# Kernel optimization log

Hardware: AMD Instinct MI355X
Metric: run time of the kernel (lower is better)

The kernel has to match this reference:

```python
import jax, jax.numpy as jnp
import numpy as np

# dims: L blocks, S cur_seq, M memory_len, B batch, D embed, H heads, IN input_dim
L, S, M, B, D, H, IN = 4, 512, 512, 8, 1024, 16, 128
HD = D // H
GRU_BIAS = 2.0  # config['gru_bias']


def _ln(x, s, b, eps=1e-5):
    mu = x.mean(-1, keepdims=True)
    var = ((x - mu) ** 2).mean(-1, keepdims=True)
    return (x - mu) * jax.lax.rsqrt(var + eps) * s + b


def _pos_emb(full_seq, dim):
    # SinusoidalPE: freqs = arange(0, dim, 2.0); inv = 10000**(-freqs/dim); seq descending
    freqs = jnp.arange(0, dim, 2.0)
    inv = 10000.0 ** (-freqs / dim)
    seq = jnp.arange(full_seq - 1, -1, -1.0)
    ang = seq[:, None] * inv[None, :]
    return jnp.concatenate([jnp.sin(ang), jnp.cos(ang)], axis=-1)  # (F, dim)


def _rel_shift(x):
    # x: (q, k, b, h) -> Transformer-XL relative shift
    q, k, b, h = x.shape
    xp = jnp.pad(x, ((0, 0), (1, 0), (0, 0), (0, 0)))
    return xp.reshape(k + 1, q, b, h)[1:].reshape(q, k, b, h)


def _gru(x, y, Wr, Ur, Wz, Uz, Wg, Ug):
    r = jax.nn.sigmoid(y @ Wr + x @ Ur)
    z = jax.nn.sigmoid(y @ Wz + x @ Uz - GRU_BIAS)
    hcand = jnp.tanh(y @ Wg + (r * x) @ Ug)
    return (1.0 - z) * x + z * hcand


def setup_inputs() -> dict:
    key = jax.random.key(0)
    ks = iter(jax.random.split(key, 64))

    def mat(*shape):
        return jax.random.normal(next(ks), shape, jnp.float32) * (shape[-2] ** -0.5)

    return dict(
        h=jax.random.normal(next(ks), (B, S, IN), jnp.float32),
        memory=jnp.zeros((L, M, B, D), jnp.float32),
        We=mat(IN, D), be=jnp.zeros((D,), jnp.float32),
        ln1_s=jnp.ones((L, D), jnp.float32), ln1_b=jnp.zeros((L, D), jnp.float32),
        ln2_s=jnp.ones((L, D), jnp.float32), ln2_b=jnp.zeros((L, D), jnp.float32),
        Wq=mat(L, D, D), bq=jnp.zeros((L, D), jnp.float32),
        Wk=mat(L, D, D), bk=jnp.zeros((L, D), jnp.float32),
        Wv=mat(L, D, D), bv=jnp.zeros((L, D), jnp.float32),
        Wr=mat(L, D, D), br=jnp.zeros((L, D), jnp.float32),
        Wo=mat(L, D, D), bo=jnp.zeros((L, D), jnp.float32),
        u=jax.random.normal(next(ks), (L, H, HD), jnp.float32) * 0.02,
        vb=jax.random.normal(next(ks), (L, H, HD), jnp.float32) * 0.02,
        gWr=mat(L, 2, D, D), gUr=mat(L, 2, D, D),
        gWz=mat(L, 2, D, D), gUz=mat(L, 2, D, D),
        gWg=mat(L, 2, D, D), gUg=mat(L, 2, D, D),
        fW1=mat(L, D, 4 * D), fb1=jnp.zeros((L, 4 * D), jnp.float32),
        fW2=mat(L, 4 * D, D), fb2=jnp.zeros((L, D), jnp.float32),
    )


def reference(h, memory, We, be, ln1_s, ln1_b, ln2_s, ln2_b,
              Wq, bq, Wk, bk, Wv, bv, Wr, br, Wo, bo, u, vb,
              gWr, gUr, gWz, gUz, gWg, gUg, fW1, fb1, fW2, fb2):
    x = jnp.transpose(h, (1, 0, 2))                      # (S, B, IN)
    x = jax.nn.gelu(x @ We + be, approximate=False)      # (S, B, D)
    F = S + M
    pos = _pos_emb(F, D)                                 # (F, D)
    mask = jnp.triu(jnp.ones((S, F), bool), k=1 + M)     # (S, F)
    scale = HD ** -0.5
    out = x
    for i in range(L):
        full = jnp.concatenate([memory[i], out], axis=0)  # (F, B, D)
        qn = _ln(out, ln1_s[i], ln1_b[i])
        kn = _ln(full, ln1_s[i], ln1_b[i])
        q = (qn @ Wq[i] + bq[i]).reshape(S, B, H, HD)
        k = (kn @ Wk[i] + bk[i]).reshape(F, B, H, HD)
        v = (kn @ Wv[i] + bv[i]).reshape(F, B, H, HD)
        r = (pos @ Wr[i] + br[i]).reshape(F, H, HD)
        content = jnp.einsum('ibhd,jbhd->ijbh', q + u[i], k)
        position = _rel_shift(jnp.einsum('ibhd,jhd->ijbh', q + vb[i], r))
        attn = (content + position) * scale               # (S, F, B, H)
        attn = jnp.where(mask[:, :, None, None], -1e30, attn)
        a = jax.nn.softmax(attn, axis=1)
        y = jnp.einsum('ijbh,jbhd->ibhd', a, v).reshape(S, B, D) @ Wo[i] + bo[i]
        y = jax.nn.gelu(y, approximate=False)
        out1 = _gru(out, y, gWr[i, 0], gUr[i, 0], gWz[i, 0], gUz[i, 0], gWg[i, 0], gUg[i, 0])
        e = _ln(out1, ln2_s[i], ln2_b[i])
        e = jax.nn.gelu(e @ fW1[i] + fb1[i], approximate=False)
        e = jax.nn.gelu(e @ fW2[i] + fb2[i], approximate=False)
        out = _gru(out1, e, gWr[i, 1], gUr[i, 1], gWz[i, 1], gUz[i, 1], gWg[i, 1], gUg[i, 1])
    return jnp.transpose(out, (1, 0, 2))                  # (B, S, D)
```

## Files before the change

kernel.cpp:

```cpp
#include <hip/hip_runtime.h>

typedef unsigned short u16;
typedef unsigned long long u64;
typedef __attribute__((ext_vector_type(8))) short bf16x8;
typedef __attribute__((ext_vector_type(4))) float f32x4;

#define DEVI __device__ __forceinline__

DEVI u16 f2b(float f) {
  unsigned u = __float_as_uint(f);
  u += 0x7fffu + ((u >> 16) & 1u);
  return (u16)(u >> 16);
}
DEVI float b2f(u16 v) { return __uint_as_float((unsigned)v << 16); }
DEVI float tanh_f(float x) {
  float xc = fminf(fmaxf(x, -15.f), 15.f);
  float e = __expf(2.f * xc);
  return (e - 1.f) / (e + 1.f);
}
DEVI float gelu_f(float x) {
  float u = 0.7978845608028654f * x * (1.f + 0.044715f * x * x);
  return 0.5f * x * (1.f + tanh_f(u));
}
DEVI float sigm_f(float x) { return 1.f / (1.f + __expf(-x)); }

DEVI void gload16(const void* g, void* l) {
  __builtin_amdgcn_global_load_lds((__attribute__((address_space(1))) void*)g,
                                   (__attribute__((address_space(3))) void*)l, 16, 0, 0);
}

template <int BN>
__global__ __launch_bounds__(256) void gemm_bt(
    const u16* __restrict__ A, const u16* __restrict__ Bt,
    const float* __restrict__ bias, float* __restrict__ C32, u16* __restrict__ C16,
    int M, int N, int K, int ldA, int ldB, int ldC,
    long long sA, long long sBb, long long sBh, long long sC, int nH, int flags)
{
  constexpr int NF = BN / 32;
  __shared__ __align__(16) u16 Sm[2][(128 + BN) * 64];
  const int z = blockIdx.z;
  const int zb = z / nH, zh = z - zb * nH;
  A  += (long long)z * sA;
  Bt += (long long)zb * sBb + (long long)zh * sBh;
  const long long cOff = (long long)z * sC;
  const int m0 = blockIdx.x * 128, n0 = blockIdx.y * BN;
  const int t = threadIdx.x, lane = t & 63;
  const int wm = ((t >> 7) & 1) * 64, wn = ((t >> 6) & 1) * (BN / 2);

  f32x4 acc[4][NF];
#pragma unroll
  for (int i = 0; i < 4; ++i)
#pragma unroll
    for (int j = 0; j < NF; ++j) { f32x4 zz = {0.f, 0.f, 0.f, 0.f}; acc[i][j] = zz; }

  auto stage = [&](int buf, int k0) {
#pragma unroll
    for (int r = 0; r < 4; ++r) {
      const int c = r * 256 + t;
      const int row = c >> 3;
      const int col = (c & 7) << 3;
      int ga = m0 + row; if (ga >= M) ga = M - 1;
      gload16(A + (long long)ga * ldA + (k0 + col),
              &Sm[buf][(size_t)(r * 256 + (t & 192)) * 8]);
    }
#pragma unroll
    for (int r = 0; r < BN / 32; ++r) {
      const int c = r * 256 + t;
      const int row = c >> 3;
      const int col = (c & 7) << 3;
      int gb = n0 + row; if (gb >= N) gb = N - 1;
      gload16(Bt + (long long)gb * ldB + (k0 + col),
              &Sm[buf][(size_t)(1024 + r * 256 + (t & 192)) * 8]);
    }
  };

  auto compute = [&](int buf) {
    const u16* As = &Sm[buf][0];
    const u16* Bs = &Sm[buf][128 * 64];
#pragma unroll
    for (int ks = 0; ks < 2; ++ks) {
      const int ko = ks * 32 + ((lane >> 4) << 3);
      bf16x8 af[4], bfv[NF];
#pragma unroll
      for (int i = 0; i < 4; ++i)
        af[i] = *(const bf16x8*)&As[(wm + i * 16 + (lane & 15)) * 64 + ko];
#pragma unroll
      for (int i = 0; i < NF; ++i)
        bfv[i] = *(const bf16x8*)&Bs[(wn + i * 16 + (lane & 15)) * 64 + ko];
#pragma unroll
      for (int mi = 0; mi < 4; ++mi)
#pragma unroll
        for (int ni = 0; ni < NF; ++ni)
          acc[mi][ni] = __builtin_amdgcn_mfma_f32_16x16x32_bf16(af[mi], bfv[ni], acc[mi][ni], 0, 0, 0);
    }
  };

  stage(0, 0);
  __syncthreads();
  int cur = 0;
  for (int k0 = 64; k0 < K; k0 += 64) {
    stage(cur ^ 1, k0);
    compute(cur);
    __syncthreads();
    cur ^= 1;
  }
  compute(cur);

  const int cb = n0 + wn + (lane & 15);
  const int rb = m0 + wm + ((lane >> 4) << 2);
#pragma unroll
  for (int ni = 0; ni < NF; ++ni) {
    const int col = cb + ni * 16;
    if (col >= N) continue;
    const float bv = (flags & 2) ? bias[col] : 0.f;
#pragma unroll
    for (int mi = 0; mi < 4; ++mi) {
#pragma unroll
      for (int q = 0; q < 4; ++q) {
        const int row = rb + mi * 16 + q;
        if (row >= M) continue;
        float x = acc[mi][ni][q] + bv;
        if (flags & 1) x = gelu_f(x);
        long long o;
        if (flags & 16)
          o = ((long long)((row & 7) * 16 + (col >> 6)) * ldC + (row >> 3)) * 64 + (col & 63);
        else if (flags & 32)
          o = ((long long)(col >> 6) * 1024 + row) * 64 + (col & 63);
        else
          o = cOff + (long long)row * ldC + col;
        if (flags & 4) C32[o] = x;
        if (flags & 8) C16[o] = f2b(x);
      }
    }
  }
}

__global__ __launch_bounds__(256) void fused_attn(
    const u16* __restrict__ Qu,
    const u16* __restrict__ Qv,
    const u16* __restrict__ Kb,
    const u16* __restrict__ Vt,
    const u16* __restrict__ Rh,
    u16* __restrict__ Y)
{
  constexpr int F = 1024;
  const int bid = blockIdx.x;
  const int wk = (bid & 7) * 128 + (bid >> 3);
  const int i0 = (wk & 7) * 64;
  const int bh = wk >> 3;
  const int h = bh & 15;

  __shared__ __align__(16) u16 QUs[64 * 64];
  __shared__ __align__(16) u16 QVs[64 * 64];
  __shared__ __align__(16) u16 Ks[64 * 64];
  __shared__ __align__(16) u16 Vs[64 * 64];
  __shared__ __align__(16) u16 Rs[64 * 64];
  __shared__ __align__(8) u16 PBT[2][64 * 68];
  __shared__ __align__(16) u16 Ps[4][16][72];

  const int t = threadIdx.x;
  const int lane = t & 63;
  const int wq = t >> 6;
  const int l15 = lane & 15, lhi = lane >> 4;

  const u16* QUg = Qu + ((size_t)bh * 512 + i0) * 64;
  const u16* QVg = Qv + ((size_t)bh * 512 + i0) * 64;
  const u16* Kg = Kb + (size_t)bh * F * 64;
  const u16* Vg = Vt + (size_t)bh * 64 * F;
  const u16* Rg = Rh + (size_t)h * F * 64;

  auto stageT = [&](const u16* g, u16* dst) {
#pragma unroll
    for (int rnd = 0; rnd < 2; ++rnd) {
      const int idx = rnd * 256 + t;
      const int row = idx >> 3;
      const int gs = (idx & 7) ^ (row & 7);
      gload16(g + row * 64 + gs * 8, dst + (size_t)(rnd * 256 + (t & 192)) * 8);
    }
  };
  auto stageVf = [&](int j0) {
#pragma unroll
    for (int rnd = 0; rnd < 2; ++rnd) {
      const int idx = rnd * 256 + t;
      const int row = idx >> 3;
      const int gs = (idx & 7) ^ (row & 7);
      gload16(Vg + (size_t)row * F + j0 + gs * 8, Vs + (size_t)(rnd * 256 + (t & 192)) * 8);
    }
  };

  stageT(QUg, QUs);
  stageT(QVg, QVs);
  const int c_lo0 = 448 - i0;
  stageT(Rg + (size_t)c_lo0 * 64, Rs);
  __syncthreads();
  {
    f32x4 pb0[4];
#pragma unroll
    for (int i = 0; i < 4; ++i) { f32x4 zz = {0.f, 0.f, 0.f, 0.f}; pb0[i] = zz; }
    __builtin_amdgcn_s_setprio(1);
#pragma unroll
    for (int ks = 0; ks < 2; ++ks) {
      const int arow = wq * 16 + l15;
      const bf16x8 av = *(const bf16x8*)&QVs[arow * 64 + (((ks * 4 + lhi) ^ (arow & 7)) << 3)];
#pragma unroll
      for (int ni = 0; ni < 4; ++ni) {
        const int brow = ni * 16 + l15;
        const bf16x8 br_ = *(const bf16x8*)&Rs[brow * 64 + (((ks * 4 + lhi) ^ (brow & 7)) << 3)];
        pb0[ni] = __builtin_amdgcn_mfma_f32_16x16x32_bf16(av, br_, pb0[ni], 0, 0, 0);
      }
    }
    __builtin_amdgcn_s_setprio(0);
#pragma unroll
    for (int ni = 0; ni < 4; ++ni) {
      u64 w = (u64)f2b(pb0[ni][0]) | ((u64)f2b(pb0[ni][1]) << 16) |
              ((u64)f2b(pb0[ni][2]) << 32) | ((u64)f2b(pb0[ni][3]) << 48);
      *(u64*)&PBT[0][(size_t)(ni * 16 + l15) * 68 + wq * 16 + lhi * 4] = w;
    }
  }

  f32x4 Oacc[4];
#pragma unroll
  for (int i = 0; i < 4; ++i) { f32x4 zz = {0.f, 0.f, 0.f, 0.f}; Oacc[i] = zz; }
  float mrow[4] = {-3.0e38f, -3.0e38f, -3.0e38f, -3.0e38f};
  float lrow[4] = {0.f, 0.f, 0.f, 0.f};

  const int nT = i0 / 64 + 9;
  for (int st = 0; st < nT; ++st) {
    const int j0 = st * 64;
    const bool lastT = (st == nT - 1);
    __syncthreads();
    stageT(Kg + (size_t)j0 * 64, Ks);
    stageVf(j0);
    if (!lastT) stageT(Rg + (size_t)(j0 - i0 + 512) * 64, Rs);
    __syncthreads();

    f32x4 cacc[4], pbh[4];
#pragma unroll
    for (int i = 0; i < 4; ++i) {
      f32x4 zz = {0.f, 0.f, 0.f, 0.f};
      cacc[i] = zz; pbh[i] = zz;
    }
    __builtin_amdgcn_s_setprio(1);
#pragma unroll
    for (int ks = 0; ks < 2; ++ks) {
      const int arow = wq * 16 + l15;
      const bf16x8 au = *(const bf16x8*)&QUs[arow * 64 + (((ks * 4 + lhi) ^ (arow & 7)) << 3)];
#pragma unroll
      for (int ni = 0; ni < 4; ++ni) {
        const int brow = ni * 16 + l15;
        const bf16x8 bk_ = *(const bf16x8*)&Ks[brow * 64 + (((ks * 4 + lhi) ^ (brow & 7)) << 3)];
        cacc[ni] = __builtin_amdgcn_mfma_f32_16x16x32_bf16(au, bk_, cacc[ni], 0, 0, 0);
      }
      if (!lastT) {
        const bf16x8 av = *(const bf16x8*)&QVs[arow * 64 + (((ks * 4 + lhi) ^ (arow & 7)) << 3)];
#pragma unroll
        for (int ni = 0; ni < 4; ++ni) {
          const int brow = ni * 16 + l15;
          const bf16x8 br_ = *(const bf16x8*)&Rs[brow * 64 + (((ks * 4 + lhi) ^ (brow & 7)) << 3)];
          pbh[ni] = __builtin_amdgcn_mfma_f32_16x16x32_bf16(av, br_, pbh[ni], 0, 0, 0);
        }
      }
    }
    __builtin_amdgcn_s_setprio(0);

    if (!lastT) {
#pragma unroll
      for (int ni = 0; ni < 4; ++ni) {
        u64 w = (u64)f2b(pbh[ni][0]) | ((u64)f2b(pbh[ni][1]) << 16) |
                ((u64)f2b(pbh[ni][2]) << 32) | ((u64)f2b(pbh[ni][3]) << 48);
        *(u64*)&PBT[(st + 1) & 1][(size_t)(ni * 16 + l15) * 68 + wq * 16 + lhi * 4] = w;
      }
    }

    const int lim = i0 - j0 + 512;
    const u16* pbLo = &PBT[st & 1][0];
    const u16* pbHi = &PBT[(st + 1) & 1][0];
    float sc[4][4];
#pragma unroll
    for (int ni = 0; ni < 4; ++ni) {
      const int dj = ni * 16 + l15;
#pragma unroll
      for (int qq = 0; qq < 4; ++qq) {
        const int di = wq * 16 + lhi * 4 + qq;
        const int cc = dj - di + 63;
        const float pb = b2f((cc < 64) ? pbLo[(size_t)cc * 68 + di]
                                       : pbHi[(size_t)(cc - 64) * 68 + di]);
        float s = (cacc[ni][qq] + pb) * 0.125f;
        if (dj - di > lim) s = -1e30f;
        sc[ni][qq] = s;
      }
    }

    float nm[4], esc[4];
#pragma unroll
    for (int qq = 0; qq < 4; ++qq) {
      float r = fmaxf(fmaxf(sc[0][qq], sc[1][qq]), fmaxf(sc[2][qq], sc[3][qq]));
      r = fmaxf(r, __shfl_xor(r, 1));
      r = fmaxf(r, __shfl_xor(r, 2));
      r = fmaxf(r, __shfl_xor(r, 4));
      r = fmaxf(r, __shfl_xor(r, 8));
      nm[qq] = fmaxf(mrow[qq], r);
      esc[qq] = __expf(mrow[qq] - nm[qq]);
      mrow[qq] = nm[qq];
    }
    float ps[4][4];
    float rsum[4] = {0.f, 0.f, 0.f, 0.f};
#pragma unroll
    for (int ni = 0; ni < 4; ++ni)
#pragma unroll
      for (int qq = 0; qq < 4; ++qq) {
        float p = __expf(sc[ni][qq] - nm[qq]);
        ps[ni][qq] = p;
        rsum[qq] += p;
      }
#pragma unroll
    for (int qq = 0; qq < 4; ++qq) {
      float r = rsum[qq];
      r += __shfl_xor(r, 1);
      r += __shfl_xor(r, 2);
      r += __shfl_xor(r, 4);
      r += __shfl_xor(r, 8);
      lrow[qq] = lrow[qq] * esc[qq] + r;
    }
#pragma unroll
    for (int nd = 0; nd < 4; ++nd)
#pragma unroll
      for (int qq = 0; qq < 4; ++qq) Oacc[nd][qq] *= esc[qq];

#pragma unroll
    for (int ni = 0; ni < 4; ++ni)
#pragma unroll
      for (int qq = 0; qq < 4; ++qq)
        Ps[wq][lhi * 4 + qq][ni * 16 + l15] = f2b(ps[ni][qq]);
    __builtin_amdgcn_s_setprio(1);
#pragma unroll
    for (int ks = 0; ks < 2; ++ks) {
      const bf16x8 pa = *(const bf16x8*)&Ps[wq][l15][ks * 32 + lhi * 8];
#pragma unroll
      for (int nd = 0; nd < 4; ++nd) {
        const int vrow = nd * 16 + l15;
        const bf16x8 vb_ = *(const bf16x8*)&Vs[vrow * 64 + (((ks * 4 + lhi) ^ (vrow & 7)) << 3)];
        Oacc[nd] = __builtin_amdgcn_mfma_f32_16x16x32_bf16(pa, vb_, Oacc[nd], 0, 0, 0);
      }
    }
    __builtin_amdgcn_s_setprio(0);
  }

  float inv[4];
#pragma unroll
  for (int qq = 0; qq < 4; ++qq) inv[qq] = 1.f / lrow[qq];
  const int b = bh >> 4;
#pragma unroll
  for (int nd = 0; nd < 4; ++nd)
#pragma unroll
    for (int qq = 0; qq < 4; ++qq) {
      const int row = i0 + wq * 16 + lhi * 4 + qq;
      const int d = nd * 16 + l15;
      Y[(size_t)row * 8192 + b * 1024 + h * 64 + d] = f2b(Oacc[nd][qq] * inv[qq]);
    }
}

__global__ __launch_bounds__(256) void biasprep(const float* __restrict__ bq,
                                                const float* __restrict__ u,
                                                const float* __restrict__ vb,
                                                float* __restrict__ bqu,
                                                float* __restrict__ dvb)
{
  const int i = blockIdx.x * 256 + threadIdx.x;
  bqu[i] = bq[i] + u[i];
  dvb[i] = vb[i] - u[i];
}

__global__ __launch_bounds__(256) void qv_make(const u16* __restrict__ QU,
                                               const float* __restrict__ dvb,
                                               u16* __restrict__ QV)
{
  const long long idx = (long long)blockIdx.x * 256 + threadIdx.x;
  const int d = idx & 63;
  const int h = (idx >> 15) & 15;
  QV[idx] = f2b(b2f(QU[idx]) + dvb[h * 64 + d]);
}

#define MAXW 20
struct WPack {
  const float* src[MAXW];
  u16* dst[MAXW];
  int K[MAXW], N[MAXW];
  int tilePrefix[MAXW + 1];
  int nm;
};

__global__ __launch_bounds__(256) void wtrans_kernel(WPack p) {
  int bid = blockIdx.x;
  int m = 0;
  while (m < p.nm && bid >= p.tilePrefix[m + 1]) ++m;
  if (m >= p.nm) return;
  const int lt = bid - p.tilePrefix[m];
  const int K = p.K[m], N = p.N[m];
  const int tN = N >> 5;
  const int kt = lt / tN, nt = lt - kt * tN;
  const int k0 = kt << 5, n0 = nt << 5;
  const float* src = p.src[m];
  u16* dst = p.dst[m];
  __shared__ float tile[32][33];
  const int t = threadIdx.x;
  const int r = t >> 3, c4 = (t & 7) << 2;
  float4 v = *(const float4*)&src[(size_t)(k0 + r) * N + n0 + c4];
  tile[r][c4 + 0] = v.x; tile[r][c4 + 1] = v.y; tile[r][c4 + 2] = v.z; tile[r][c4 + 3] = v.w;
  __syncthreads();
  u16 o0 = f2b(tile[c4 + 0][r]);
  u16 o1 = f2b(tile[c4 + 1][r]);
  u16 o2 = f2b(tile[c4 + 2][r]);
  u16 o3 = f2b(tile[c4 + 3][r]);
  u64 w = (u64)o0 | ((u64)o1 << 16) | ((u64)o2 << 32) | ((u64)o3 << 48);
  *(u64*)&dst[(size_t)(n0 + r) * K + k0 + c4] = w;
}

__global__ __launch_bounds__(256) void ln_kernel(
    const float* __restrict__ Xmem, const float* __restrict__ Xout, int rowsMem,
    const float* __restrict__ sc, const float* __restrict__ bi, u16* __restrict__ dst)
{
  const int row = blockIdx.x;
  const float* src = (row < rowsMem) ? (Xmem + (long long)row * 1024)
                                     : (Xout + (long long)(row - rowsMem) * 1024);
  const int t = threadIdx.x;
  float4 v = *(const float4*)&src[t * 4];
  float s1 = v.x + v.y + v.z + v.w;
  float s2 = v.x * v.x + v.y * v.y + v.z * v.z + v.w * v.w;
#pragma unroll
  for (int o = 32; o > 0; o >>= 1) { s1 += __shfl_down(s1, o); s2 += __shfl_down(s2, o); }
  __shared__ float red[8];
  const int wv = t >> 6;
  if ((t & 63) == 0) { red[wv * 2] = s1; red[wv * 2 + 1] = s2; }
  __syncthreads();
  s1 = red[0] + red[2] + red[4] + red[6];
  s2 = red[1] + red[3] + red[5] + red[7];
  const float mu = s1 * (1.f / 1024.f);
  const float var = s2 * (1.f / 1024.f) - mu * mu;
  const float rs = rsqrtf(var + 1e-5f);
  float vals[4] = {v.x, v.y, v.z, v.w};
  u16 o4[4];
#pragma unroll
  for (int j = 0; j < 4; ++j) {
    const int c = t * 4 + j;
    o4[j] = f2b((vals[j] - mu) * rs * sc[c] + bi[c]);
  }
  *(u64*)&dst[(long long)row * 1024 + t * 4] =
      (u64)o4[0] | ((u64)o4[1] << 16) | ((u64)o4[2] << 32) | ((u64)o4[3] << 48);
}

__global__ __launch_bounds__(256) void prep_vt16(const u16* __restrict__ Vf, u16* __restrict__ VT)
{
  const int f0 = blockIdx.x * 64;
  const int bh = blockIdx.y;
  const int b = bh >> 4, h = bh & 15;
  __shared__ u16 tl[64 * 64];
  const int t = threadIdx.x;
  {
    const int fr = t >> 2, c0 = (t & 3) * 16;
    const u16* src = Vf + ((size_t)(f0 + fr) * 8 + b) * 1024 + h * 64 + c0;
    *(bf16x8*)&tl[fr * 64 + c0] = *(const bf16x8*)src;
    *(bf16x8*)&tl[fr * 64 + c0 + 8] = *(const bf16x8*)(src + 8);
  }
  __syncthreads();
  {
    const int dr = t >> 2, c0 = (t & 3) * 16;
    u16* dst = VT + ((long long)bh * 64 + dr) * 1024 + f0 + c0;
#pragma unroll
    for (int j = 0; j < 16; ++j) dst[j] = tl[(c0 + j) * 64 + dr];
  }
}

__global__ __launch_bounds__(256) void pe_kernel(u16* __restrict__ PEB)
{
  const long long idx = (long long)blockIdx.x * 256 + threadIdx.x;
  const int p = (int)(idx >> 10);
  const int d = idx & 1023;
  const int q = d & 511;
  const float inv = powf(10000.f, -(float)(2 * q) * (1.f / 1024.f));
  const float ang = (float)(1023 - p) * inv;
  PEB[idx] = f2b((d < 512) ? sinf(ang) : cosf(ang));
}

__global__ __launch_bounds__(256) void embed_conv(const float* __restrict__ h, u16* __restrict__ A)
{
  const long long idx = (long long)blockIdx.x * 256 + threadIdx.x;
  const int c = idx & 127;
  const int r = (int)(idx >> 7);
  const int s = r >> 3, b = r & 7;
  A[idx] = f2b(h[(((long long)b * 512 + s) << 7) + c]);
}

__global__ __launch_bounds__(256) void gru_elemA(const float* __restrict__ T1, float* __restrict__ T2,
                                                 const float* __restrict__ X, u16* __restrict__ RXBF)
{
  const long long i4 = ((long long)blockIdx.x * 256 + threadIdx.x) * 4;
  const int row = (int)(i4 >> 10);
  const int c = i4 & 1023;
  const float* t1 = T1 + (long long)row * 3072 + c;
  float* t2 = T2 + (long long)row * 2048 + c;
  float4 ry = *(const float4*)t1;
  float4 zy = *(const float4*)(t1 + 1024);
  float4 rx = *(const float4*)t2;
  float4 zx = *(const float4*)(t2 + 1024);
  float4 x = *(const float4*)(X + i4);
  float rr[4], zz[4];
  rr[0] = sigm_f(ry.x + rx.x); rr[1] = sigm_f(ry.y + rx.y);
  rr[2] = sigm_f(ry.z + rx.z); rr[3] = sigm_f(ry.w + rx.w);
  zz[0] = sigm_f(zy.x + zx.x - 2.f); zz[1] = sigm_f(zy.y + zx.y - 2.f);
  zz[2] = sigm_f(zy.z + zx.z - 2.f); zz[3] = sigm_f(zy.w + zx.w - 2.f);
  u16 o4[4];
  o4[0] = f2b(rr[0] * x.x); o4[1] = f2b(rr[1] * x.y);
  o4[2] = f2b(rr[2] * x.z); o4[3] = f2b(rr[3] * x.w);
  *(u64*)&RXBF[i4] = (u64)o4[0] | ((u64)o4[1] << 16) | ((u64)o4[2] << 32) | ((u64)o4[3] << 48);
  float4 zo; zo.x = zz[0]; zo.y = zz[1]; zo.z = zz[2]; zo.w = zz[3];
  *(float4*)t2 = zo;
}

__global__ __launch_bounds__(256) void gru_elemB(const float* __restrict__ T1, const float* __restrict__ T2,
                                                 const float* __restrict__ TG, const float* __restrict__ X,
                                                 float* __restrict__ O, u16* __restrict__ XBF)
{
  const long long i4 = ((long long)blockIdx.x * 256 + threadIdx.x) * 4;
  const int row = (int)(i4 >> 10);
  const int c = i4 & 1023;
  float4 gy = *(const float4*)(T1 + (long long)row * 3072 + 2048 + c);
  float4 tt = *(const float4*)(TG + i4);
  float4 z = *(const float4*)(T2 + (long long)row * 2048 + c);
  float4 x = *(const float4*)(X + i4);
  float4 o;
  o.x = (1.f - z.x) * x.x + z.x * tanh_f(gy.x + tt.x);
  o.y = (1.f - z.y) * x.y + z.y * tanh_f(gy.y + tt.y);
  o.z = (1.f - z.z) * x.z + z.z * tanh_f(gy.z + tt.z);
  o.w = (1.f - z.w) * x.w + z.w * tanh_f(gy.w + tt.w);
  *(float4*)(O + i4) = o;
  u16 o4[4];
  o4[0] = f2b(o.x); o4[1] = f2b(o.y); o4[2] = f2b(o.z); o4[3] = f2b(o.w);
  *(u64*)&XBF[i4] = (u64)o4[0] | ((u64)o4[1] << 16) | ((u64)o4[2] << 32) | ((u64)o4[3] << 48);
}

__global__ __launch_bounds__(256) void out_transpose(const float* __restrict__ O, float* __restrict__ dst)
{
  const long long i4 = ((long long)blockIdx.x * 256 + threadIdx.x) * 4;
  const int d = i4 & 1023;
  const int r = (int)(i4 >> 10);
  const int s = r >> 3, b = r & 7;
  float4 v = *(const float4*)(O + i4);
  *(float4*)&dst[(((long long)b * 512 + s) << 10) + d] = v;
}

extern "C" void kernel_launch(void* const* d_in, const int* in_sizes, int n_in,
                              void* d_out, int out_size, void* d_ws, size_t ws_size,
                              hipStream_t stream)
{
  (void)in_sizes; (void)n_in; (void)out_size; (void)ws_size;
  const float* h_in   = (const float*)d_in[0];
  const float* memory = (const float*)d_in[1];
  const float* We     = (const float*)d_in[2];
  const float* be     = (const float*)d_in[3];
  const float* ln1s   = (const float*)d_in[4];
  const float* ln1b   = (const float*)d_in[5];
  const float* ln2s   = (const float*)d_in[6];
  const float* ln2b   = (const float*)d_in[7];
  const float* Wq     = (const float*)d_in[8];
  const float* bq     = (const float*)d_in[9];
  const float* Wk     = (const float*)d_in[10];
  const float* bk     = (const float*)d_in[11];
  const float* Wv     = (const float*)d_in[12];
  const float* bv     = (const float*)d_in[13];
  const float* Wr     = (const float*)d_in[14];
  const float* br     = (const float*)d_in[15];
  const float* Wo     = (const float*)d_in[16];
  const float* bo     = (const float*)d_in[17];
  const float* uu     = (const float*)d_in[18];
  const float* vbp    = (const float*)d_in[19];
  const float* gWr    = (const float*)d_in[20];
  const float* gUr    = (const float*)d_in[21];
  const float* gWz    = (const float*)d_in[22];
  const float* gUz    = (const float*)d_in[23];
  const float* gWg    = (const float*)d_in[24];
  const float* gUg    = (const float*)d_in[25];
  const float* fW1    = (const float*)d_in[26];
  const float* fb1    = (const float*)d_in[27];
  const float* fW2    = (const float*)d_in[28];
  const float* fb2    = (const float*)d_in[29];

  constexpr int S = 512, MM = 512, B = 8, D = 1024, H = 16, IN = 128, F = 1024;
  constexpr int SB = 4096, FB = 8192;
  constexpr long long DD = (long long)D * D;

  char* ws = (char*)d_ws;
  size_t off = 0;
  auto alloc = [&](size_t bytes) -> size_t {
    size_t o = off; off = (off + bytes + 255) & ~(size_t)255; return o;
  };
  const size_t oWT   = alloc((size_t)25 * DD * 2);
  const size_t oWET  = alloc((size_t)D * IN * 2);
  const size_t oPEB  = alloc((size_t)F * D * 2);
  const size_t oOUT  = alloc((size_t)SB * D * 4);
  const size_t oOUT1 = alloc((size_t)SB * D * 4);
  const size_t oXBF  = alloc((size_t)SB * D * 2);
  const size_t oYBF  = alloc((size_t)SB * D * 2);
  const size_t oYBFA = alloc((size_t)SB * D * 2);
  const size_t oABUF = alloc((size_t)SB * D * 2);
  const size_t oKN   = alloc((size_t)FB * D * 2);
  const size_t oQU   = alloc((size_t)B * H * S * 64 * 2);
  const size_t oQV   = alloc((size_t)B * H * S * 64 * 2);
  const size_t oKBH  = alloc((size_t)B * H * F * 64 * 2);
  const size_t oVT   = alloc((size_t)B * H * F * 64 * 2);
  const size_t oRH   = alloc((size_t)H * F * 64 * 2);
  const size_t oBQU  = alloc((size_t)D * 4);
  const size_t oDVB  = alloc((size_t)D * 4);
  const size_t oUNI  = off;

  u16* WTp   = (u16*)(ws + oWT);
  u16* WETp  = (u16*)(ws + oWET);
  u16* PEBp  = (u16*)(ws + oPEB);
  float* OUTp  = (float*)(ws + oOUT);
  float* OUT1p = (float*)(ws + oOUT1);
  u16* XBFp  = (u16*)(ws + oXBF);
  u16* YBFp  = (u16*)(ws + oYBF);
  u16* YBFAp = (u16*)(ws + oYBFA);
  u16* ABUFp = (u16*)(ws + oABUF);
  u16* KNp   = (u16*)(ws + oKN);
  u16* QUp   = (u16*)(ws + oQU);
  u16* QVp   = (u16*)(ws + oQV);
  u16* KBHp  = (u16*)(ws + oKBH);
  u16* VTp   = (u16*)(ws + oVT);
  u16* RHp   = (u16*)(ws + oRH);
  float* bquP = (float*)(ws + oBQU);
  float* dvbP = (float*)(ws + oDVB);
  u16* VF16p  = (u16*)(ws + oUNI);
  float* T1   = (float*)(ws + oUNI);
  float* T2   = (float*)(ws + oUNI + (size_t)SB * 3 * D * 4);
  float* TGp  = (float*)(ws + oUNI + (size_t)SB * 5 * D * 4);
  u16* FFNBp  = (u16*)(ws + oUNI);

  auto gemm = [&](const u16* A, const u16* Bt, const float* bias, float* C32, u16* C16,
                  int M, int N, int K, int ldA, int ldB, int ldC,
                  long long sA, long long sBb, long long sBh, long long sC, int nH, int Z,
                  int flags) {
    if (N <= 1024) {
      dim3 grid((M + 127) / 128, (N + 63) / 64, Z);
      gemm_bt<64><<<grid, 256, 0, stream>>>(A, Bt, bias, C32, C16, M, N, K, ldA, ldB, ldC,
                                            sA, sBb, sBh, sC, nH, flags);
    } else {
      dim3 grid((M + 127) / 128, (N + 127) / 128, Z);
      gemm_bt<128><<<grid, 256, 0, stream>>>(A, Bt, bias, C32, C16, M, N, K, ldA, ldB, ldC,
                                             sA, sBb, sBh, sC, nH, flags);
    }
  };

  pe_kernel<<<(F * D) / 256, 256, 0, stream>>>(PEBp);
  {
    WPack p{};
    p.nm = 1; p.src[0] = We; p.dst[0] = WETp; p.K[0] = IN; p.N[0] = D;
    p.tilePrefix[0] = 0; p.tilePrefix[1] = (IN / 32) * (D / 32);
    wtrans_kernel<<<p.tilePrefix[1], 256, 0, stream>>>(p);
  }
  embed_conv<<<(SB * IN) / 256, 256, 0, stream>>>(h_in, ABUFp);
  gemm(ABUFp, WETp, be, OUTp, XBFp, SB, D, IN, IN, IN, D, 0, 0, 0, 0, 1, 1, 1 | 2 | 4 | 8);

  for (int li = 0; li < 4; ++li) {
    WPack p{};
    int nt = 0, id = 0;
    auto addw = [&](const float* s, u16* d, int K, int N) {
      p.src[id] = s; p.dst[id] = d; p.K[id] = K; p.N[id] = N;
      p.tilePrefix[id] = nt; nt += (K / 32) * (N / 32); ++id;
    };
    addw(Wq + li * DD, WTp + 0 * DD, D, D);
    addw(Wk + li * DD, WTp + 1 * DD, D, D);
    addw(Wv + li * DD, WTp + 2 * DD, D, D);
    addw(Wr + li * DD, WTp + 3 * DD, D, D);
    addw(Wo + li * DD, WTp + 4 * DD, D, D);
    addw(gWr + (li * 2 + 0) * DD, WTp + 5 * DD, D, D);
    addw(gWz + (li * 2 + 0) * DD, WTp + 6 * DD, D, D);
    addw(gWg + (li * 2 + 0) * DD, WTp + 7 * DD, D, D);
    addw(gUr + (li * 2 + 0) * DD, WTp + 8 * DD, D, D);
    addw(gUz + (li * 2 + 0) * DD, WTp + 9 * DD, D, D);
    addw(gUg + (li * 2 + 0) * DD, WTp + 10 * DD, D, D);
    addw(gWr + (li * 2 + 1) * DD, WTp + 11 * DD, D, D);
    addw(gWz + (li * 2 + 1) * DD, WTp + 12 * DD, D, D);
    addw(gWg + (li * 2 + 1) * DD, WTp + 13 * DD, D, D);
    addw(gUr + (li * 2 + 1) * DD, WTp + 14 * DD, D, D);
    addw(gUz + (li * 2 + 1) * DD, WTp + 15 * DD, D, D);
    addw(gUg + (li * 2 + 1) * DD, WTp + 16 * DD, D, D);
    addw(fW1 + li * (long long)D * 4096, WTp + 17 * DD, D, 4096);
    addw(fW2 + li * (long long)4096 * D, WTp + 21 * DD, 4096, D);
    p.tilePrefix[id] = nt; p.nm = id;
    wtrans_kernel<<<nt, 256, 0, stream>>>(p);

    ln_kernel<<<FB, 256, 0, stream>>>(memory + (long long)li * MM * B * D, OUTp, MM * B,
                                      ln1s + li * D, ln1b + li * D, KNp);
    const u16* QN = KNp + (size_t)MM * B * D;

    biasprep<<<4, 256, 0, stream>>>(bq + li * D, uu + li * D, vbp + li * D, bquP, dvbP);
    gemm(QN, WTp + 0 * DD, bquP, nullptr, QUp, SB, D, D, D, D,  S,
         0, 0, 0, 0, 1, 1, 2 | 8 | 16);
    qv_make<<<(B * H * S * 64) / 256, 256, 0, stream>>>(QUp, dvbP, QVp);
    gemm(KNp, WTp + 1 * DD, bk + li * D, nullptr, KBHp, FB, D, D, D, D,  F,
         0, 0, 0, 0, 1, 1, 2 | 8 | 16);
    gemm(KNp, WTp + 2 * DD, bv + li * D, nullptr, VF16p, FB, D, D, D, D, D,
         0, 0, 0, 0, 1, 1, 2 | 8);
    prep_vt16<<<dim3(F / 64, B * H), 256, 0, stream>>>(VF16p, VTp);
    gemm(PEBp, WTp + 3 * DD, br + li * D, nullptr, RHp, F, D, D, D, D, D,
         0, 0, 0, 0, 1, 1, 2 | 8 | 32);

    fused_attn<<<dim3((S / 64) * B * H), 256, 0, stream>>>(QUp, QVp, KBHp, VTp, RHp, YBFAp);

    gemm(YBFAp, WTp + 4 * DD, bo + li * D, nullptr, YBFp, SB, D, D, D, D, D, 0, 0, 0, 0, 1, 1, 1 | 2 | 8);

    gemm(YBFp, WTp + 5 * DD, nullptr, T1, nullptr, SB, 3 * D, D, D, D, 3 * D, 0, 0, 0, 0, 1, 1, 4);
    gemm(XBFp, WTp + 8 * DD, nullptr, T2, nullptr, SB, 2 * D, D, D, D, 2 * D, 0, 0, 0, 0, 1, 1, 4);
    gru_elemA<<<(SB * D / 4) / 256, 256, 0, stream>>>(T1, T2, OUTp, ABUFp);
    gemm(ABUFp, WTp + 10 * DD, nullptr, TGp, nullptr, SB, D, D, D, D, D, 0, 0, 0, 0, 1, 1, 4);
    gru_elemB<<<(SB * D / 4) / 256, 256, 0, stream>>>(T1, T2, TGp, OUTp, OUT1p, XBFp);

    ln_kernel<<<SB, 256, 0, stream>>>(OUT1p, OUT1p, SB, ln2s + li * D, ln2b + li * D, ABUFp);
    gemm(ABUFp, WTp + 17 * DD, fb1 + li * 4096, nullptr, FFNBp, SB, 4096, D, D, D, 4096,
         0, 0, 0, 0, 1, 1, 1 | 2 | 8);
    gemm(FFNBp, WTp + 21 * DD, fb2 + li * D, nullptr, YBFp, SB, D, 4096, 4096, 4096, D,
         0, 0, 0, 0, 1, 1, 1 | 2 | 8);

    gemm(YBFp, WTp + 11 * DD, nullptr, T1, nullptr, SB, 3 * D, D, D, D, 3 * D, 0, 0, 0, 0, 1, 1, 4);
    gemm(XBFp, WTp + 14 * DD, nullptr, T2, nullptr, SB, 2 * D, D, D, D, 2 * D, 0, 0, 0, 0, 1, 1, 4);
    gru_elemA<<<(SB * D / 4) / 256, 256, 0, stream>>>(T1, T2, OUT1p, ABUFp);
    gemm(ABUFp, WTp + 16 * DD, nullptr, TGp, nullptr, SB, D, D, D, D, D, 0, 0, 0, 0, 1, 1, 4);
    gru_elemB<<<(SB * D / 4) / 256, 256, 0, stream>>>(T1, T2, TGp, OUT1p, OUTp, XBFp);
  }

  out_transpose<<<(SB * D / 4) / 256, 256, 0, stream>>>(OUTp, (float*)d_out);
}
```

Before: 3.141 ms.

## Double-buffer attention K/V/R tiles and fuse QV and K/V projection GEMMs

The fused attention kernel now double-buffers the K, V and R tiles in shared memory so the loads for the next tile overlap compute on the current one. Q fragments are held in registers instead of shared memory, and the softmax uses exp2 with the log2e factor folded into the scale. On the host side, the qv_make kernel is removed because the Q GEMM epilogue writes both QU and QV, and the K and V projections run as one batched GEMM launch with per-z bias and output selection. These changes cut launches and intermediate traffic but add epilogue branching and more shared-memory use per block.

New measurement: 3.289 ms. +4.7%, slower.

```diff
diff --git a/kernel.cpp b/kernel.cpp
--- a/kernel.cpp
+++ b/kernel.cpp
@@ -32,7 +32,8 @@
 template <int BN>
 __global__ __launch_bounds__(256) void gemm_bt(
     const u16* __restrict__ A, const u16* __restrict__ Bt,
-    const float* __restrict__ bias, float* __restrict__ C32, u16* __restrict__ C16,
+    const float* __restrict__ bias, const float* __restrict__ bias2,
+    float* __restrict__ C32, u16* __restrict__ C16, u16* __restrict__ C16b,
     int M, int N, int K, int ldA, int ldB, int ldC,
     long long sA, long long sBb, long long sBh, long long sC, int nH, int flags)
 {
@@ -112,7 +113,8 @@
   for (int ni = 0; ni < NF; ++ni) {
     const int col = cb + ni * 16;
     if (col >= N) continue;
-    const float bv = (flags & 2) ? bias[col] : 0.f;
+    float bv = 0.f;
+    if (flags & 2) bv = ((flags & 128) && zh) ? bias2[col] : bias[col];
 #pragma unroll
     for (int mi = 0; mi < 4; ++mi) {
 #pragma unroll
@@ -121,15 +123,28 @@
         if (row >= M) continue;
         float x = acc[mi][ni][q] + bv;
         if (flags & 1) x = gelu_f(x);
-        long long o;
-        if (flags & 16)
-          o = ((long long)((row & 7) * 16 + (col >> 6)) * ldC + (row >> 3)) * 64 + (col & 63);
-        else if (flags & 32)
-          o = ((long long)(col >> 6) * 1024 + row) * 64 + (col & 63);
-        else
-          o = cOff + (long long)row * ldC + col;
-        if (flags & 4) C32[o] = x;
-        if (flags & 8) C16[o] = f2b(x);
+        if (flags & 64) {
+          const long long o = ((long long)((row & 7) * 16 + (col >> 6)) * ldC + (row >> 3)) * 64 + (col & 63);
+          C16[o] = f2b(x);
+          C16b[o] = f2b(x + bias2[col]);
+        } else if (flags & 128) {
+          if (zh == 0) {
+            const long long o = ((long long)((row & 7) * 16 + (col >> 6)) * ldC + (row >> 3)) * 64 + (col & 63);
+            C16[o] = f2b(x);
+          } else {
+            C16b[(long long)row * 1024 + col] = f2b(x);
+          }
+        } else {
+          long long o;
+          if (flags & 16)
+            o = ((long long)((row & 7) * 16 + (col >> 6)) * ldC + (row >> 3)) * 64 + (col & 63);
+          else if (flags & 32)
+            o = ((long long)(col >> 6) * 1024 + row) * 64 + (col & 63);
+          else
+            o = cOff + (long long)row * ldC + col;
+          if (flags & 4) C32[o] = x;
+          if (flags & 8) C16[o] = f2b(x);
+        }
       }
     }
   }
@@ -144,17 +159,16 @@
     u16* __restrict__ Y)
 {
   constexpr int F = 1024;
+  constexpr float KSC = 0.1803368801111244f;
   const int bid = blockIdx.x;
   const int wk = (bid & 7) * 128 + (bid >> 3);
   const int i0 = (wk & 7) * 64;
   const int bh = wk >> 3;
   const int h = bh & 15;
 
-  __shared__ __align__(16) u16 QUs[64 * 64];
-  __shared__ __align__(16) u16 QVs[64 * 64];
-  __shared__ __align__(16) u16 Ks[64 * 64];
-  __shared__ __align__(16) u16 Vs[64 * 64];
-  __shared__ __align__(16) u16 Rs[64 * 64];
+  __shared__ __align__(16) u16 Ks[2][64 * 64];
+  __shared__ __align__(16) u16 Vs[2][64 * 64];
+  __shared__ __align__(16) u16 Rs[2][64 * 64];
   __shared__ __align__(8) u16 PBT[2][64 * 68];
   __shared__ __align__(16) u16 Ps[4][16][72];
 
@@ -169,6 +183,14 @@
   const u16* Vg = Vt + (size_t)bh * 64 * F;
   const u16* Rg = Rh + (size_t)h * F * 64;
 
+  bf16x8 au[2], av[2];
+#pragma unroll
+  for (int ks = 0; ks < 2; ++ks) {
+    const int arow = wq * 16 + l15;
+    au[ks] = *(const bf16x8*)(QUg + arow * 64 + ks * 32 + lhi * 8);
+    av[ks] = *(const bf16x8*)(QVg + arow * 64 + ks * 32 + lhi * 8);
+  }
+
   auto stageT = [&](const u16* g, u16* dst) {
 #pragma unroll
     for (int rnd = 0; rnd < 2; ++rnd) {
@@ -178,20 +200,22 @@
       gload16(g + row * 64 + gs * 8, dst + (size_t)(rnd * 256 + (t & 192)) * 8);
     }
   };
-  auto stageVf = [&](int j0) {
+  auto stageVf = [&](int j0, u16* dst) {
 #pragma unroll
     for (int rnd = 0; rnd < 2; ++rnd) {
       const int idx = rnd * 256 + t;
       const int row = idx >> 3;
       const int gs = (idx & 7) ^ (row & 7);
-      gload16(Vg + (size_t)row * F + j0 + gs * 8, Vs + (size_t)(rnd * 256 + (t & 192)) * 8);
+      gload16(Vg + (size_t)row * F + j0 + gs * 8, dst + (size_t)(rnd * 256 + (t & 192)) * 8);
     }
   };
 
-  stageT(QUg, QUs);
-  stageT(QVg, QVs);
-  const int c_lo0 = 448 - i0;
-  stageT(Rg + (size_t)c_lo0 * 64, Rs);
+  const int nT = i0 / 64 + 9;
+
+  stageT(Kg, Ks[0]);
+  stageVf(0, Vs[0]);
+  stageT(Rg + (size_t)(512 - i0) * 64, Rs[0]);
+  stageT(Rg + (size_t)(448 - i0) * 64, Rs[1]);
   __syncthreads();
   {
     f32x4 pb0[4];
@@ -199,16 +223,13 @@
     for (int i = 0; i < 4; ++i) { f32x4 zz = {0.f, 0.f, 0.f, 0.f}; pb0[i] = zz; }
     __builtin_amdgcn_s_setprio(1);
 #pragma unroll
-    for (int ks = 0; ks < 2; ++ks) {
-      const int arow = wq * 16 + l15;
-      const bf16x8 av = *(const bf16x8*)&QVs[arow * 64 + (((ks * 4 + lhi) ^ (arow & 7)) << 3)];
+    for (int ks = 0; ks < 2; ++ks)
 #pragma unroll
       for (int ni = 0; ni < 4; ++ni) {
         const int brow = ni * 16 + l15;
-        const bf16x8 br_ = *(const bf16x8*)&Rs[brow * 64 + (((ks * 4 + lhi) ^ (brow & 7)) << 3)];
-        pb0[ni] = __builtin_amdgcn_mfma_f32_16x16x32_bf16(av, br_, pb0[ni], 0, 0, 0);
+        const bf16x8 br_ = *(const bf16x8*)&Rs[1][brow * 64 + (((ks * 4 + lhi) ^ (brow & 7)) << 3)];
+        pb0[ni] = __builtin_amdgcn_mfma_f32_16x16x32_bf16(av[ks], br_, pb0[ni], 0, 0, 0);
       }
-    }
     __builtin_amdgcn_s_setprio(0);
 #pragma unroll
     for (int ni = 0; ni < 4; ++ni) {
@@ -217,6 +238,7 @@
       *(u64*)&PBT[0][(size_t)(ni * 16 + l15) * 68 + wq * 16 + lhi * 4] = w;
     }
   }
+  __syncthreads();
 
   f32x4 Oacc[4];
 #pragma unroll
@@ -224,15 +246,17 @@
   float mrow[4] = {-3.0e38f, -3.0e38f, -3.0e38f, -3.0e38f};
   float lrow[4] = {0.f, 0.f, 0.f, 0.f};
 
-  const int nT = i0 / 64 + 9;
   for (int st = 0; st < nT; ++st) {
-    const int j0 = st * 64;
+    const int b = st & 1;
     const bool lastT = (st == nT - 1);
-    __syncthreads();
-    stageT(Kg + (size_t)j0 * 64, Ks);
-    stageVf(j0);
-    if (!lastT) stageT(Rg + (size_t)(j0 - i0 + 512) * 64, Rs);
-    __syncthreads();
+
+    if (!lastT) {
+      const int j1 = (st + 1) * 64;
+      stageT(Kg + (size_t)j1 * 64, Ks[b ^ 1]);
+      stageVf(j1, Vs[b ^ 1]);
+      if (st + 1 < nT - 1)
+        stageT(Rg + (size_t)(j1 - i0 + 512) * 64, Rs[b ^ 1]);
+    }
 
     f32x4 cacc[4], pbh[4];
 #pragma unroll
@@ -243,21 +267,18 @@
     __builtin_amdgcn_s_setprio(1);
 #pragma unroll
     for (int ks = 0; ks < 2; ++ks) {
-      const int arow = wq * 16 + l15;
-      const bf16x8 au = *(const bf16x8*)&QUs[arow * 64 + (((ks * 4 + lhi) ^ (arow & 7)) << 3)];
 #pragma unroll
       for (int ni = 0; ni < 4; ++ni) {
         const int brow = ni * 16 + l15;
-        const bf16x8 bk_ = *(const bf16x8*)&Ks[brow * 64 + (((ks * 4 + lhi) ^ (brow & 7)) << 3)];
-        cacc[ni] = __builtin_amdgcn_mfma_f32_16x16x32_bf16(au, bk_, cacc[ni], 0, 0, 0);
+        const bf16x8 bk_ = *(const bf16x8*)&Ks[b][brow * 64 + (((ks * 4 + lhi) ^ (brow & 7)) << 3)];
+        cacc[ni] = __builtin_amdgcn_mfma_f32_16x16x32_bf16(au[ks], bk_, cacc[ni], 0, 0, 0);
       }
       if (!lastT) {
-        const bf16x8 av = *(const bf16x8*)&QVs[arow * 64 + (((ks * 4 + lhi) ^ (arow & 7)) << 3)];
 #pragma unroll
         for (int ni = 0; ni < 4; ++ni) {
           const int brow = ni * 16 + l15;
-          const bf16x8 br_ = *(const bf16x8*)&Rs[brow * 64 + (((ks * 4 + lhi) ^ (brow & 7)) << 3)];
-          pbh[ni] = __builtin_amdgcn_mfma_f32_16x16x32_bf16(av, br_, pbh[ni], 0, 0, 0);
+          const bf16x8 br_ = *(const bf16x8*)&Rs[b][brow * 64 + (((ks * 4 + lhi) ^ (brow & 7)) << 3)];
+          pbh[ni] = __builtin_amdgcn_mfma_f32_16x16x32_bf16(av[ks], br_, pbh[ni], 0, 0, 0);
         }
       }
     }
@@ -272,7 +293,6 @@
       }
     }
 
-    const int lim = i0 - j0 + 512;
     const u16* pbLo = &PBT[st & 1][0];
     const u16* pbHi = &PBT[(st + 1) & 1][0];
     float sc[4][4];
@@ -285,8 +305,8 @@
         const int cc = dj - di + 63;
         const float pb = b2f((cc < 64) ? pbLo[(size_t)cc * 68 + di]
                                        : pbHi[(size_t)(cc - 64) * 68 + di]);
-        float s = (cacc[ni][qq] + pb) * 0.125f;
-        if (dj - di > lim) s = -1e30f;
+        float s = (cacc[ni][qq] + pb) * KSC;
+        if (lastT && dj > di) s = -1e30f;
         sc[ni][qq] = s;
       }
     }
@@ -300,7 +320,7 @@
       r = fmaxf(r, __shfl_xor(r, 4));
       r = fmaxf(r, __shfl_xor(r, 8));
       nm[qq] = fmaxf(mrow[qq], r);
-      esc[qq] = __expf(mrow[qq] - nm[qq]);
+      esc[qq] = exp2f(mrow[qq] - nm[qq]);
       mrow[qq] = nm[qq];
     }
     float ps[4][4];
@@ -309,7 +329,7 @@
     for (int ni = 0; ni < 4; ++ni)
 #pragma unroll
       for (int qq = 0; qq < 4; ++qq) {
-        float p = __expf(sc[ni][qq] - nm[qq]);
+        float p = exp2f(sc[ni][qq] - nm[qq]);
         ps[ni][qq] = p;
         rsum[qq] += p;
       }
@@ -339,11 +359,13 @@
 #pragma unroll
       for (int nd = 0; nd < 4; ++nd) {
         const int vrow = nd * 16 + l15;
-        const bf16x8 vb_ = *(const bf16x8*)&Vs[vrow * 64 + (((ks * 4 + lhi) ^ (vrow & 7)) << 3)];
+        const bf16x8 vb_ = *(const bf16x8*)&Vs[b][vrow * 64 + (((ks * 4 + lhi) ^ (vrow & 7)) << 3)];
         Oacc[nd] = __builtin_amdgcn_mfma_f32_16x16x32_bf16(pa, vb_, Oacc[nd], 0, 0, 0);
       }
     }
     __builtin_amdgcn_s_setprio(0);
+
+    __syncthreads();
   }
 
   float inv[4];
@@ -369,16 +391,6 @@
   const int i = blockIdx.x * 256 + threadIdx.x;
   bqu[i] = bq[i] + u[i];
   dvb[i] = vb[i] - u[i];
-}
-
-__global__ __launch_bounds__(256) void qv_make(const u16* __restrict__ QU,
-                                               const float* __restrict__ dvb,
-                                               u16* __restrict__ QV)
-{
-  const long long idx = (long long)blockIdx.x * 256 + threadIdx.x;
-  const int d = idx & 63;
-  const int h = (idx >> 15) & 15;
-  QV[idx] = f2b(b2f(QU[idx]) + dvb[h * 64 + d]);
 }
 
 #define MAXW 20
@@ -636,17 +648,20 @@
   float* TGp  = (float*)(ws + oUNI + (size_t)SB * 5 * D * 4);
   u16* FFNBp  = (u16*)(ws + oUNI);
 
-  auto gemm = [&](const u16* A, const u16* Bt, const float* bias, float* C32, u16* C16,
+  auto gemm = [&](const u16* A, const u16* Bt, const float* bias, const float* bias2,
+                  float* C32, u16* C16, u16* C16b,
                   int M, int N, int K, int ldA, int ldB, int ldC,
                   long long sA, long long sBb, long long sBh, long long sC, int nH, int Z,
                   int flags) {
     if (N <= 1024) {
       dim3 grid((M + 127) / 128, (N + 63) / 64, Z);
-      gemm_bt<64><<<grid, 256, 0, stream>>>(A, Bt, bias, C32, C16, M, N, K, ldA, ldB, ldC,
+      gemm_bt<64><<<grid, 256, 0, stream>>>(A, Bt, bias, bias2, C32, C16, C16b,
+                                            M, N, K, ldA, ldB, ldC,
                                             sA, sBb, sBh, sC, nH, flags);
     } else {
       dim3 grid((M + 127) / 128, (N + 127) / 128, Z);
-      gemm_bt<128><<<grid, 256, 0, stream>>>(A, Bt, bias, C32, C16, M, N, K, ldA, ldB, ldC,
+      gemm_bt<128><<<grid, 256, 0, stream>>>(A, Bt, bias, bias2, C32, C16, C16b,
+                                             M, N, K, ldA, ldB, ldC,
                                              sA, sBb, sBh, sC, nH, flags);
     }
   };
@@ -659,7 +674,8 @@
     wtrans_kernel<<<p.tilePrefix[1], 256, 0, stream>>>(p);
   }
   embed_conv<<<(SB * IN) / 256, 256, 0, stream>>>(h_in, ABUFp);
-  gemm(ABUFp, WETp, be, OUTp, XBFp, SB, D, IN, IN, IN, D, 0, 0, 0, 0, 1, 1, 1 | 2 | 4 | 8);
+  gemm(ABUFp, WETp, be, nullptr, OUTp, XBFp, nullptr, SB, D, IN, IN, IN, D,
+       0, 0, 0, 0, 1, 1, 1 | 2 | 4 | 8);
 
   for (int li = 0; li < 4; ++li) {
     WPack p{};
@@ -695,37 +711,41 @@
     const u16* QN = KNp + (size_t)MM * B * D;
 
     biasprep<<<4, 256, 0, stream>>>(bq + li * D, uu + li * D, vbp + li * D, bquP, dvbP);
-    gemm(QN, WTp + 0 * DD, bquP, nullptr, QUp, SB, D, D, D, D,  S,
-         0, 0, 0, 0, 1, 1, 2 | 8 | 16);
-    qv_make<<<(B * H * S * 64) / 256, 256, 0, stream>>>(QUp, dvbP, QVp);
-    gemm(KNp, WTp + 1 * DD, bk + li * D, nullptr, KBHp, FB, D, D, D, D,  F,
-         0, 0, 0, 0, 1, 1, 2 | 8 | 16);
-    gemm(KNp, WTp + 2 * DD, bv + li * D, nullptr, VF16p, FB, D, D, D, D, D,
-         0, 0, 0, 0, 1, 1, 2 | 8);
+    gemm(QN, WTp + 0 * DD, bquP, dvbP, nullptr, QUp, QVp, SB, D, D, D, D,  S,
+         0, 0, 0, 0, 1, 1, 2 | 64);
+    gemm(KNp, WTp + 1 * DD, bk + li * D, bv + li * D, nullptr, KBHp, VF16p,
+         FB, D, D, D, D,  F, 0, 0, DD, 0, 2, 2, 2 | 128);
     prep_vt16<<<dim3(F / 64, B * H), 256, 0, stream>>>(VF16p, VTp);
-    gemm(PEBp, WTp + 3 * DD, br + li * D, nullptr, RHp, F, D, D, D, D, D,
-         0, 0, 0, 0, 1, 1, 2 | 8 | 32);
+    gemm(PEBp, WTp + 3 * DD, br + li * D, nullptr, nullptr, RHp, nullptr,
+         F, D, D, D, D, D, 0, 0, 0, 0, 1, 1, 2 | 8 | 32);
 
     fused_attn<<<dim3((S / 64) * B * H), 256, 0, stream>>>(QUp, QVp, KBHp, VTp, RHp, YBFAp);
 
-    gemm(YBFAp, WTp + 4 * DD, bo + li * D, nullptr, YBFp, SB, D, D, D, D, D, 0, 0, 0, 0, 1, 1, 1 | 2 | 8);
-
-    gemm(YBFp, WTp + 5 * DD, nullptr, T1, nullptr, SB, 3 * D, D, D, D, 3 * D, 0, 0, 0, 0, 1, 1, 4);
-    gemm(XBFp, WTp + 8 * DD, nullptr, T2, nullptr, SB, 2 * D, D, D, D, 2 * D, 0, 0, 0, 0, 1, 1, 4);
+    gemm(YBFAp, WTp + 4 * DD, bo + li * D, nullptr, nullptr, YBFp, nullptr,
+         SB, D, D, D, D, D, 0, 0, 0, 0, 1, 1, 1 | 2 | 8);
+
+    gemm(YBFp, WTp + 5 * DD, nullptr, nullptr, T1, nullptr, nullptr,
+         SB, 3 * D, D, D, D, 3 * D, 0, 0, 0, 0, 1, 1, 4);
+    gemm(XBFp, WTp + 8 * DD, nullptr, nullptr, T2, nullptr, nullptr,
+         SB, 2 * D, D, D, D, 2 * D, 0, 0, 0, 0, 1, 1, 4);
     gru_elemA<<<(SB * D / 4) / 256, 256, 0, stream>>>(T1, T2, OUTp, ABUFp);
-    gemm(ABUFp, WTp + 10 * DD, nullptr, TGp, nullptr, SB, D, D, D, D, D, 0, 0, 0, 0, 1, 1, 4);
+    gemm(ABUFp, WTp + 10 * DD, nullptr, nullptr, TGp, nullptr, nullptr,
+         SB, D, D, D, D, D, 0, 0, 0, 0, 1, 1, 4);
     gru_elemB<<<(SB * D / 4) / 256, 256, 0, stream>>>(T1, T2, TGp, OUTp, OUT1p, XBFp);
 
     ln_kernel<<<SB, 256, 0, stream>>>(OUT1p, OUT1p, SB, ln2s + li * D, ln2b + li * D, ABUFp);
-    gemm(ABUFp, WTp + 17 * DD, fb1 + li * 4096, nullptr, FFNBp, SB, 4096, D, D, D, 4096,
-         0, 0, 0, 0, 1, 1, 1 | 2 | 8);
-    gemm(FFNBp, WTp + 21 * DD, fb2 + li * D, nullptr, YBFp, SB, D, 4096, 4096, 4096, D,
-         0, 0, 0, 0, 1, 1, 1 | 2 | 8);
-
-    gemm(YBFp, WTp + 11 * DD, nullptr, T1, nullptr, SB, 3 * D, D, D, D, 3 * D, 0, 0, 0, 0, 1, 1, 4);
-    gemm(XBFp, WTp + 14 * DD, nullptr, T2, nullptr, SB, 2 * D, D, D, D, 2 * D, 0, 0, 0, 0, 1, 1, 4);
+    gemm(ABUFp, WTp + 17 * DD, fb1 + li * 4096, nullptr, nullptr, FFNBp, nullptr,
+         SB, 4096, D, D, D, 4096, 0, 0, 0, 0, 1, 1, 1 | 2 | 8);
+    gemm(FFNBp, WTp + 21 * DD, fb2 + li * D, nullptr, nullptr, YBFp, nullptr,
+         SB, D, 4096, 4096, 4096, D, 0, 0, 0, 0, 1, 1, 1 | 2 | 8);
+
+    gemm(YBFp, WTp + 11 * DD, nullptr, nullptr, T1, nullptr, nullptr,
+         SB, 3 * D, D, D, D, 3 * D, 0, 0, 0, 0, 1, 1, 4);
+    gemm(XBFp, WTp + 14 * DD, nullptr, nullptr, T2, nullptr, nullptr,
+         SB, 2 * D, D, D, D, 2 * D, 0, 0, 0, 0, 1, 1, 4);
     gru_elemA<<<(SB * D / 4) / 256, 256, 0, stream>>>(T1, T2, OUT1p, ABUFp);
-    gemm(ABUFp, WTp + 16 * DD, nullptr, TGp, nullptr, SB, D, D, D, D, D, 0, 0, 0, 0, 1, 1, 4);
+    gemm(ABUFp, WTp + 16 * DD, nullptr, nullptr, TGp, nullptr, nullptr,
+         SB, D, D, D, D, D, 0, 0, 0, 0, 1, 1, 4);
     gru_elemB<<<(SB * D / 4) / 256, 256, 0, stream>>>(T1, T2, TGp, OUT1p, OUTp, XBFp);
   }
 
```
